# Kernel optimization log

Hardware: AMD Instinct MI355X
Metric: run time of the kernel (lower is better)

The kernel has to match this reference:

```python
import jax, jax.numpy as jnp
import numpy as np

B, S, D, H = 4, 1024, 1024, 16
HS = D // H  # head_size = 64


def setup_inputs() -> dict:
    key = jax.random.key(0)
    ks = jax.random.split(key, 12)
    sc_d = 1.0 / np.sqrt(D)
    sc_h = 1.0 / np.sqrt(HS)
    inp = {
        "queries": jax.random.normal(ks[0], (B, S, D), jnp.float32),
        "keys": jax.random.normal(ks[1], (B, S, D), jnp.float32),
        "values": jax.random.normal(ks[2], (B, S, D), jnp.float32),
        # causal mask: scores where mask == 0 are filled with -1e9
        "mask": jnp.tril(jnp.ones((S, S), jnp.int32)),
        # per-head query/key projections: [H, D, HS] weights, [H, HS] biases
        "Wq": jax.random.uniform(ks[3], (H, D, HS), jnp.float32, -sc_d, sc_d),
        "bq": jax.random.uniform(ks[4], (H, HS), jnp.float32, -sc_d, sc_d),
        "Wk": jax.random.uniform(ks[5], (H, D, HS), jnp.float32, -sc_d, sc_d),
        "bk": jax.random.uniform(ks[6], (H, HS), jnp.float32, -sc_d, sc_d),
        # shared value projection: [D, HS]
        "Wv": jax.random.uniform(ks[7], (D, HS), jnp.float32, -sc_d, sc_d),
        "bv": jax.random.uniform(ks[8], (HS,), jnp.float32, -sc_d, sc_d),
        # output projection: [HS, D]
        "Wo": jax.random.uniform(ks[9], (HS, D), jnp.float32, -sc_h, sc_h),
        "bo": jax.random.uniform(ks[10], (D,), jnp.float32, -sc_h, sc_h),
    }
    return inp


def reference(queries, keys, values, mask, Wq, bq, Wk, bk, Wv, bv, Wo, bo):
    # shared value projection: [B, S, HS]
    v = jnp.einsum("bsd,de->bse", values, Wv) + bv
    # batched per-head projections (replaces the python loop over heads)
    q = jnp.einsum("bsd,hde->bhse", queries, Wq) + bq[None, :, None, :]
    k = jnp.einsum("btd,hde->bhte", keys, Wk) + bk[None, :, None, :]
    scores = jnp.einsum("bhse,bhte->bhst", q, k) / jnp.sqrt(jnp.float32(HS))
    scores = jnp.where(mask == 0, jnp.float32(-1e9), scores)
    attn = jax.nn.softmax(scores, axis=-1)  # [B, H, S, S]; dropout = eval-mode identity
    head_out = jnp.einsum("bhst,bte->bhse", attn, v)
    out = head_out.mean(axis=1)  # mean over heads -> [B, S, HS]
    out = jnp.einsum("bse,ed->bsd", out, Wo) + bo
    attention_weights = attn.mean(axis=1)  # [B, S, S]
    return out, attention_weights
```

## Files before the change

kernel.cpp:

```cpp
#include <hip/hip_runtime.h>
#include <hip/hip_bf16.h>
#include <stdint.h>

typedef _Float16 half8 __attribute__((ext_vector_type(8)));
typedef _Float16 half4 __attribute__((ext_vector_type(4)));
typedef float    f32x4 __attribute__((ext_vector_type(4)));

#define MFMA16(a, b, c) __builtin_amdgcn_mfma_f32_16x16x32_f16(a, b, c, 0, 0, 0)

typedef __attribute__((address_space(1))) const void GVOID;
typedef __attribute__((address_space(3))) void LVOID;
__device__ __forceinline__ void glds16(const void* g, void* l)
{
    __builtin_amdgcn_global_load_lds((GVOID*)g, (LVOID*)l, 16, 0, 0);
}

#define BARRIER() do { asm volatile("" ::: "memory"); \
    __builtin_amdgcn_s_barrier(); \
    asm volatile("" ::: "memory"); } while (0)

__global__ __launch_bounds__(256) void prep_all(
    const float* __restrict__ Wq, const float* __restrict__ Wk,
    const float* __restrict__ Wv, const float* __restrict__ Wo,
    const float* __restrict__ queries, const float* __restrict__ keys,
    _Float16* __restrict__ WqkT, _Float16* __restrict__ WvT,
    _Float16* __restrict__ WoT, _Float16* __restrict__ a16,
    float* __restrict__ ctx, float* __restrict__ attn)
{
    __shared__ float t[32][33];
    const int id = blockIdx.x;
    const int tid = threadIdx.x;

    if (id < 2176) {
        const float* X; _Float16* Y; int R, C, bx, by;
        if (id < 2048) {
            const int isK = id >> 10;
            const int local = id & 1023;
            bx = local & 1;
            by = (local >> 1) & 31;
            const int hz = local >> 6;
            X = (isK ? Wk : Wq) + (long)hz * 65536;
            Y = WqkT + (long)isK * 1048576 + (long)hz * 65536;
            R = 1024; C = 64;
        } else if (id < 2112) {
            const int local = id - 2048;
            bx = local & 1; by = local >> 1;
            X = Wv; Y = WvT; R = 1024; C = 64;
        } else {
            const int local = id - 2112;
            bx = local & 31; by = local >> 5;
            X = Wo; Y = WoT; R = 64; C = 1024;
        }
        const int c0 = bx * 32, r0 = by * 32;
        const int tx = tid & 31, ty = tid >> 5;
#pragma unroll
        for (int i = 0; i < 4; ++i)
            t[ty + i * 8][tx] = X[(long)(r0 + ty + i * 8) * C + c0 + tx];
        __syncthreads();
#pragma unroll
        for (int i = 0; i < 4; ++i)
            Y[(long)(c0 + ty + i * 8) * R + r0 + tx] = (_Float16)t[tx][ty + i * 8];
    } else if (id < 6272) {
        const int isK = (id - 2176) >> 11;
        const int local = (id - 2176) & 2047;
        const float* S = isK ? keys : queries;
        _Float16* Dz = a16 + (long)isK * 4194304;
        const long i = ((long)local * 256 + tid) * 8;
        const float4 v0 = *(const float4*)(S + i);
        const float4 v1 = *(const float4*)(S + i + 4);
        half8 h;
        h[0] = (_Float16)v0.x; h[1] = (_Float16)v0.y;
        h[2] = (_Float16)v0.z; h[3] = (_Float16)v0.w;
        h[4] = (_Float16)v1.x; h[5] = (_Float16)v1.y;
        h[6] = (_Float16)v1.z; h[7] = (_Float16)v1.w;
        *(half8*)(Dz + i) = h;
    } else if (id < 6528) {
        const float4 z = {0.f, 0.f, 0.f, 0.f};
        ((float4*)ctx)[(long)(id - 6272) * 256 + tid] = z;
    } else {
        const float4 z = {0.f, 0.f, 0.f, 0.f};
        ((float4*)attn)[(long)(id - 6528) * 256 + tid] = z;
    }
}

__global__ __launch_bounds__(256, 2) void qk_vproj(
    const _Float16* __restrict__ A16,
    const _Float16* __restrict__ BT,
    const float* __restrict__ bias0, const float* __restrict__ bias1,
    _Float16* __restrict__ Cout,
    const float* __restrict__ values,
    const _Float16* __restrict__ WvT,
    const float* __restrict__ bv,
    _Float16* __restrict__ vT)
{
    __shared__ __align__(16) char smem[65536];
    const int lid = blockIdx.x;
    const int tid = threadIdx.x;
    const int wave = tid >> 6, lane = tid & 63;
    const int m16  = lane & 15, quad = lane >> 4;

    if (lid < 32) {
        _Float16 (*As)[72] = (_Float16(*)[72])smem;
        _Float16 (*Bs)[72] = (_Float16(*)[72])(smem + 128 * 72 * 2);
        const int mt = lid;
        const int m0 = mt * 128;

        const int acol = (tid & 15) * 4;
        const int arb  = tid >> 4;
        const int bj   = tid >> 1;
        const int bcc  = (tid & 1) * 32;
        const int jn = (bj > 63) ? 63 : bj;
        const _Float16* bpB = WvT + (long)jn * 1024;

        f32x4 acc[2][8];
        {
            f32x4 zz = {0.f, 0.f, 0.f, 0.f};
#pragma unroll
            for (int i = 0; i < 2; ++i)
#pragma unroll
                for (int j = 0; j < 8; ++j) acc[i][j] = zz;
        }

        for (int k0 = 0; k0 < 1024; k0 += 64) {
            {
                float4 av[8];
#pragma unroll
                for (int p = 0; p < 8; ++p)
                    av[p] = *(const float4*)(values + (long)(m0 + arb + p * 16) * 1024 + k0 + acol);
#pragma unroll
                for (int p = 0; p < 8; ++p) {
                    half4 hv;
                    hv[0] = (_Float16)av[p].x; hv[1] = (_Float16)av[p].y;
                    hv[2] = (_Float16)av[p].z; hv[3] = (_Float16)av[p].w;
                    *(half4*)&As[arb + p * 16][acol] = hv;
                }
            }
            {
                const _Float16* bp = bpB + k0 + bcc;
                half8 b0 = *(const half8*)(bp);
                half8 b1 = *(const half8*)(bp + 8);
                half8 b2 = *(const half8*)(bp + 16);
                half8 b3 = *(const half8*)(bp + 24);
                *(half8*)&Bs[bj][bcc]      = b0;
                *(half8*)&Bs[bj][bcc + 8]  = b1;
                *(half8*)&Bs[bj][bcc + 16] = b2;
                *(half8*)&Bs[bj][bcc + 24] = b3;
            }
            __syncthreads();
#pragma unroll
            for (int kss = 0; kss < 2; ++kss) {
                const int ko = kss * 32 + quad * 8;
                const half8 a0 = *(const half8*)&As[wave * 32 + m16][ko];
                const half8 a1 = *(const half8*)&As[wave * 32 + 16 + m16][ko];
#pragma unroll
                for (int c = 0; c < 4; ++c) {
                    const half8 bf = *(const half8*)&Bs[c * 16 + m16][ko];
                    acc[0][c] = MFMA16(a0, bf, acc[0][c]);
                    acc[1][c] = MFMA16(a1, bf, acc[1][c]);
                }
            }
            __syncthreads();
        }

#pragma unroll
        for (int hh = 0; hh < 2; ++hh) {
#pragma unroll
            for (int c = 0; c < 4; ++c) {
                const int e  = c * 16 + m16;
                const float bb = bv[e];
#pragma unroll
                for (int r = 0; r < 4; ++r) {
                    const int row = m0 + wave * 32 + hh * 16 + quad * 4 + r;
                    const int b = row >> 10, tt = row & 1023;
                    vT[(long)b * 65536 + (long)e * 1024 + tt] =
                        (_Float16)(acc[hh][c][r] + bb);
                }
            }
        }
        return;
    }

    const int lid2 = lid - 32;
    const int xcd = lid2 & 7, loc = lid2 >> 3;
    const int sw  = xcd * 64 + loc;
    const int nt  = sw & 7;
    const int tm2 = sw >> 3;
    const int mt  = tm2 & 31;
    const int z   = tm2 >> 5;

    const int n0 = nt * 128;
    const int m0 = mt * 128;

    const char* Az = (const char*)(A16 + (long)z * 4194304);
    const char* Bz = (const char*)(BT  + (long)z * 1048576);

    const int colbyte = (((lane & 7) ^ (lane >> 3)) << 4);
    const char* gaBase = Az + ((long)(m0 + wave * 32 + (lane >> 3)) << 11) + colbyte;
    const char* gbBase = Bz + ((long)(n0 + wave * 32 + (lane >> 3)) << 11) + colbyte;

    f32x4 acc[2][8];
    {
        f32x4 zz = {0.f, 0.f, 0.f, 0.f};
#pragma unroll
        for (int i = 0; i < 2; ++i)
#pragma unroll
            for (int j = 0; j < 8; ++j) acc[i][j] = zz;
    }

    auto STAGE = [&](int bf, int k0) {
        const char* ga = gaBase + (k0 << 1);
        const char* gb = gbBase + (k0 << 1);
        _Float16* la = (_Float16*)(smem + bf * 16384) + wave * 32 * 64;
        _Float16* lb = (_Float16*)(smem + 32768 + bf * 16384) + wave * 32 * 64;
#pragma unroll
        for (int i = 0; i < 4; ++i) {
            glds16(ga + (long)i * 8 * 2048, la + i * 8 * 64);
            glds16(gb + (long)i * 8 * 2048, lb + i * 8 * 64);
        }
    };

    auto COMPUTE = [&](int bf) {
        const char* Ab = smem + bf * 16384;
        const char* Bp = smem + 32768 + bf * 16384;
        const int sw4 = (m16 & 7) << 4;
#pragma unroll
        for (int kss = 0; kss < 2; ++kss) {
            const int kbs = (kss * 64 + quad * 16) ^ sw4;
            const half8 a0 = *(const half8*)(Ab + (wave * 32 + m16) * 128 + kbs);
            const half8 a1 = *(const half8*)(Ab + (wave * 32 + 16 + m16) * 128 + kbs);
#pragma unroll
            for (int c = 0; c < 8; ++c) {
                const half8 bfr = *(const half8*)(Bp + (c * 16 + m16) * 128 + kbs);
                acc[0][c] = MFMA16(a0, bfr, acc[0][c]);
                acc[1][c] = MFMA16(a1, bfr, acc[1][c]);
            }
        }
    };

    STAGE(0, 0);
    STAGE(1, 64);
    int cur = 0;
    for (int t = 0; t < 15; ++t) {
        asm volatile("s_waitcnt vmcnt(8)" ::: "memory");
        __builtin_amdgcn_sched_barrier(0);
        BARRIER();
        COMPUTE(cur);
        BARRIER();
        if (t < 14) STAGE(cur, (t + 2) * 64);
        cur ^= 1;
    }
    asm volatile("s_waitcnt vmcnt(0)" ::: "memory");
    __builtin_amdgcn_sched_barrier(0);
    BARRIER();
    COMPUTE(cur);

    const float* bias = z ? bias1 : bias0;
    _Float16* Cz = Cout + (long)z * 4194304;
#pragma unroll
    for (int hh = 0; hh < 2; ++hh) {
#pragma unroll
        for (int c = 0; c < 8; ++c) {
            const int col = n0 + c * 16 + m16;
            const float bb = bias[col];
#pragma unroll
            for (int r = 0; r < 4; ++r) {
                const int row = m0 + wave * 32 + hh * 16 + quad * 4 + r;
                Cz[(long)row * 1024 + col] = (_Float16)(acc[hh][c][r] + bb);
            }
        }
    }
}

__global__ __launch_bounds__(256, 2) void gemm_f16_v2(
    const float* __restrict__ A0, const float* __restrict__ A1,
    const _Float16* __restrict__ BT,
    const float* __restrict__ bias0, const float* __restrict__ bias1,
    void* __restrict__ Cout,
    int N, int lda, int ldbt, int ldc,
    long aBS, long bBS, long cBS,
    int c_half, int atomic, int nks, int kchunk)
{
    __shared__ __align__(16) _Float16 As[128][72];
    __shared__ __align__(16) _Float16 Bs[128][72];

    const int gx  = gridDim.x, gy = gridDim.y;
    const int nwg = gx * gy * (int)gridDim.z;
    const int lid = (int)blockIdx.x + gx * ((int)blockIdx.y + gy * (int)blockIdx.z);
    const int q8  = nwg >> 3, r8 = nwg & 7;
    const int xcd = lid & 7, loc = lid >> 3;
    const int sw  = (xcd < r8 ? xcd * (q8 + 1) : r8 * (q8 + 1) + (xcd - r8) * q8) + loc;
    const int nt  = sw % gx;
    const int tm2 = sw / gx;
    const int mt  = tm2 % gy;
    const int bz  = tm2 / gy;

    const int b = bz / nks, ks = bz % nks;
    const int kbeg = ks * kchunk;
    const int kend = kbeg + kchunk;

    const float* A = A1 ? (b ? A1 : A0) : (A0 + (long)b * aBS);
    const _Float16* Bb = BT + (long)b * bBS;

    const int n0 = nt * 128;
    const int m0 = mt * 128;
    const int tid  = threadIdx.x;
    const int wave = tid >> 6, lane = tid & 63;
    const int m16  = lane & 15, quad = lane >> 4;

    const int acol = (tid & 15) * 4;
    const int arb  = tid >> 4;
    const int bj   = tid >> 1;
    const int bcc  = (tid & 1) * 32;
    int jn = n0 + bj; if (jn > N - 1) jn = N - 1;
    const _Float16* bpB = Bb + (long)jn * ldbt;

    f32x4 acc[2][8];
    {
        f32x4 zz = {0.f, 0.f, 0.f, 0.f};
#pragma unroll
        for (int i = 0; i < 2; ++i)
#pragma unroll
            for (int j = 0; j < 8; ++j) acc[i][j] = zz;
    }

    for (int k0 = kbeg; k0 < kend; k0 += 64) {
        {
            float4 av[8];
#pragma unroll
            for (int p = 0; p < 8; ++p)
                av[p] = *(const float4*)(A + (long)(m0 + arb + p * 16) * lda + k0 + acol);
#pragma unroll
            for (int p = 0; p < 8; ++p) {
                half4 hv;
                hv[0] = (_Float16)av[p].x; hv[1] = (_Float16)av[p].y;
                hv[2] = (_Float16)av[p].z; hv[3] = (_Float16)av[p].w;
                *(half4*)&As[arb + p * 16][acol] = hv;
            }
        }
        {
            const _Float16* bp = bpB + k0 + bcc;
            half8 b0 = *(const half8*)(bp);
            half8 b1 = *(const half8*)(bp + 8);
            half8 b2 = *(const half8*)(bp + 16);
            half8 b3 = *(const half8*)(bp + 24);
            *(half8*)&Bs[bj][bcc]      = b0;
            *(half8*)&Bs[bj][bcc + 8]  = b1;
            *(half8*)&Bs[bj][bcc + 16] = b2;
            *(half8*)&Bs[bj][bcc + 24] = b3;
        }
        __syncthreads();
#pragma unroll
        for (int kss = 0; kss < 2; ++kss) {
            const int ko = kss * 32 + quad * 8;
            const half8 a0 = *(const half8*)&As[wave * 32 + m16][ko];
            const half8 a1 = *(const half8*)&As[wave * 32 + 16 + m16][ko];
#pragma unroll
            for (int c = 0; c < 8; ++c) {
                const half8 bf = *(const half8*)&Bs[c * 16 + m16][ko];
                acc[0][c] = MFMA16(a0, bf, acc[0][c]);
                acc[1][c] = MFMA16(a1, bf, acc[1][c]);
            }
        }
        __syncthreads();
    }

    const float* bias = b ? bias1 : bias0;
    const int addb = (bias != nullptr) && (kbeg == 0);
#pragma unroll
    for (int hh = 0; hh < 2; ++hh) {
#pragma unroll
        for (int c = 0; c < 8; ++c) {
            const int col = n0 + c * 16 + m16;
            if (col >= N) continue;
            const float bb = addb ? bias[col] : 0.f;
#pragma unroll
            for (int r = 0; r < 4; ++r) {
                const int row = m0 + wave * 32 + hh * 16 + quad * 4 + r;
                const float v = acc[hh][c][r] + bb;
                const long idx = (long)b * cBS + (long)row * ldc + col;
                if (atomic)      atomicAdd(&((float*)Cout)[idx], v);
                else if (c_half) ((_Float16*)Cout)[idx] = (_Float16)v;
                else             ((float*)Cout)[idx] = v;
            }
        }
    }
}

__global__ __launch_bounds__(256, 4) void attn_stats(
    const _Float16* __restrict__ q_all, const _Float16* __restrict__ k_all,
    float* __restrict__ m_out, float* __restrict__ il_out)
{
    const int st = blockIdx.x, h = blockIdx.y, b = blockIdx.z;
    const int tid = threadIdx.x, wave = tid >> 6, lane = tid & 63;
    const int m16 = lane & 15, quad = lane >> 4;
    const int s0 = st * 64;
    const int sw = s0 + wave * 16;

    __shared__ __align__(16) _Float16 qs[64][72];
    __shared__ __align__(16) _Float16 ks[128][72];

    const int srow = tid >> 2;
    const int scol = (tid & 3) * 16;

    {
        const _Float16* qsrc = q_all + ((long)(b * 1024 + s0 + srow)) * 1024 + h * 64 + scol;
        *(half8*)&qs[srow][scol]     = *(const half8*)(qsrc);
        *(half8*)&qs[srow][scol + 8] = *(const half8*)(qsrc + 8);
    }

    const _Float16* ksrcb = k_all + ((long)(b * 1024 + srow)) * 1024 + h * 64 + scol;

    float mr[4], lr[4];
#pragma unroll
    for (int r = 0; r < 4; ++r) { mr[r] = -3.0e38f; lr[r] = 0.f; }

    half8 a0, a1;
    for (int ch = 0; 2 * ch <= st; ++ch) {
        const int tbase = 2 * ch;
        const int two = (tbase + 1 <= st);

        const _Float16* ksrc0 = ksrcb + (long)(tbase * 64) * 1024;
        const half8 k0 = *(const half8*)(ksrc0);
        const half8 k1 = *(const half8*)(ksrc0 + 8);
        half8 k2, k3;
        if (two) {
            const _Float16* ksrc1 = ksrc0 + (long)64 * 1024;
            k2 = *(const half8*)(ksrc1);
            k3 = *(const half8*)(ksrc1 + 8);
        }

        __syncthreads();
        *(half8*)&ks[srow][scol]     = k0;
        *(half8*)&ks[srow][scol + 8] = k1;
        if (two) {
            *(half8*)&ks[64 + srow][scol]     = k2;
            *(half8*)&ks[64 + srow][scol + 8] = k3;
        }
        __syncthreads();

        if (ch == 0) {
            a0 = *(const half8*)&qs[wave * 16 + m16][quad * 8];
            a1 = *(const half8*)&qs[wave * 16 + m16][quad * 8 + 32];
        }

        const int ncol = two ? 8 : 4;
        for (int c = 0; c < ncol; ++c) {
            const half8 b0 = *(const half8*)&ks[c * 16 + m16][quad * 8];
            const half8 b1 = *(const half8*)&ks[c * 16 + m16][quad * 8 + 32];
            f32x4 cc = {0.f, 0.f, 0.f, 0.f};
            cc = MFMA16(a0, b0, cc);
            cc = MFMA16(a1, b1, cc);
            const int tile = tbase + (c >> 2);
            if (tile < st) {
#pragma unroll
                for (int r = 0; r < 4; ++r) {
                    const float zz = cc[r] * 0.125f;
                    const float nm = fmaxf(mr[r], zz);
                    lr[r] = lr[r] * __expf(mr[r] - nm) + __expf(zz - nm);
                    mr[r] = nm;
                }
            } else {
                const int col = tile * 64 + (c & 3) * 16 + m16;
#pragma unroll
                for (int r = 0; r < 4; ++r) {
                    const int row = sw + quad * 4 + r;
                    if (col <= row) {
                        const float zz = cc[r] * 0.125f;
                        const float nm = fmaxf(mr[r], zz);
                        lr[r] = lr[r] * __expf(mr[r] - nm) + __expf(zz - nm);
                        mr[r] = nm;
                    }
                }
            }
        }
    }

#pragma unroll
    for (int mk = 1; mk < 16; mk <<= 1) {
#pragma unroll
        for (int r = 0; r < 4; ++r) {
            const float om = __shfl_xor(mr[r], mk);
            const float ol = __shfl_xor(lr[r], mk);
            const float nm = fmaxf(mr[r], om);
            lr[r] = lr[r] * __expf(mr[r] - nm) + ol * __expf(om - nm);
            mr[r] = nm;
        }
    }
    if (m16 == 0) {
#pragma unroll
        for (int r = 0; r < 4; ++r) {
            const long idx = ((long)(b * 16 + h)) * 1024 + sw + quad * 4 + r;
            m_out[idx]  = mr[r];
            il_out[idx] = 1.f / lr[r];
        }
    }
}

__global__ __launch_bounds__(256, 4) void attn_pmean(
    const _Float16* __restrict__ q_all, const _Float16* __restrict__ k_all,
    const float* __restrict__ m_in, const float* __restrict__ il_in,
    const _Float16* __restrict__ vT,
    float* __restrict__ attn,
    float* __restrict__ ctx)
{
    const int ttile = blockIdx.x, stile = blockIdx.y, b = blockIdx.z;
    const int tid = threadIdx.x;
    if (ttile > stile) return;

    __shared__ __align__(16) _Float16 qs2[2][64 * 64];
    __shared__ __align__(16) _Float16 ks2[2][64 * 64];
    __shared__ __align__(16) float mls[16][64];
    __shared__ __align__(16) float ils[16][64];

    const int wave = tid >> 6, lane = tid & 63;
    const int m16 = lane & 15, quad = lane >> 4;
    const int s0 = stile * 64;
    const int t0 = ttile * 64;
    const int sw = s0 + wave * 16;
    const int diag = (ttile == stile);

    {
        const int hh = tid >> 4;
        const int c4 = (tid & 15) * 4;
        const long ix = ((long)(b * 16 + hh)) * 1024 + s0 + c4;
        const float4 mv4 = *(const float4*)&m_in[ix];
        const float4 iv4 = *(const float4*)&il_in[ix];
        *(float4*)&mls[hh][c4] = mv4;
        *(float4*)&ils[hh][c4] = iv4;
    }

    const int colb = (((lane & 7) ^ (lane >> 3)) << 4);
    const char* gq = (const char*)q_all + ((long)(b * 1024 + s0 + wave * 16 + (lane >> 3)) << 11) + colb;
    const char* gk = (const char*)k_all + ((long)(b * 1024 + t0 + wave * 16 + (lane >> 3)) << 11) + colb;

    auto STAGE_P = [&](int bf, int h) {
        const char* q = gq + h * 128;
        const char* k = gk + h * 128;
        _Float16* lq = &qs2[bf][wave * 16 * 64];
        _Float16* lk = &ks2[bf][wave * 16 * 64];
        glds16(q, lq);
        glds16(q + 8 * 2048, lq + 8 * 64);
        glds16(k, lk);
        glds16(k + 8 * 2048, lk + 8 * 64);
    };

    STAGE_P(0, 0);
    STAGE_P(1, 1);
    asm volatile("s_waitcnt lgkmcnt(0)" ::: "memory");
    BARRIER();

    float pm[4][4];
#pragma unroll
    for (int c = 0; c < 4; ++c)
#pragma unroll
        for (int r = 0; r < 4; ++r) pm[c][r] = 0.f;

    const int swz = (m16 & 7) << 4;
    int cur = 0;

    auto COMPUTE_H = [&](int h, int bf) {
        const char* Qc = (const char*)&qs2[bf][0];
        const char* Kc = (const char*)&ks2[bf][0];
        const half8 a0 = *(const half8*)(Qc + (wave * 16 + m16) * 128 + ((quad * 16) ^ swz));
        const half8 a1 = *(const half8*)(Qc + (wave * 16 + m16) * 128 + ((quad * 16 + 64) ^ swz));
        const float4 mv = *(const float4*)&mls[h][wave * 16 + quad * 4];
        const float4 iv = *(const float4*)&ils[h][wave * 16 + quad * 4];
        const float mrow[4] = {mv.x, mv.y, mv.z, mv.w};
        const float irow[4] = {iv.x, iv.y, iv.z, iv.w};
        if (!diag) {
#pragma unroll
            for (int c = 0; c < 4; ++c) {
                const half8 b0 = *(const half8*)(Kc + (c * 16 + m16) * 128 + ((quad * 16) ^ swz));
                const half8 b1 = *(const half8*)(Kc + (c * 16 + m16) * 128 + ((quad * 16 + 64) ^ swz));
                f32x4 cc = {0.f, 0.f, 0.f, 0.f};
                cc = MFMA16(a0, b0, cc);
                cc = MFMA16(a1, b1, cc);
#pragma unroll
                for (int r = 0; r < 4; ++r)
                    pm[c][r] += __expf(cc[r] * 0.125f - mrow[r]) * irow[r];
            }
        } else {
#pragma unroll
            for (int c = 0; c < 4; ++c) {
                const half8 b0 = *(const half8*)(Kc + (c * 16 + m16) * 128 + ((quad * 16) ^ swz));
                const half8 b1 = *(const half8*)(Kc + (c * 16 + m16) * 128 + ((quad * 16 + 64) ^ swz));
                f32x4 cc = {0.f, 0.f, 0.f, 0.f};
                cc = MFMA16(a0, b0, cc);
                cc = MFMA16(a1, b1, cc);
                const int col = t0 + c * 16 + m16;
#pragma unroll
                for (int r = 0; r < 4; ++r) {
                    const int row = sw + quad * 4 + r;
                    if (col <= row)
                        pm[c][r] += __expf(cc[r] * 0.125f - mrow[r]) * irow[r];
                }
            }
        }
    };

    for (int h = 0; h < 15; ++h) {
        asm volatile("s_waitcnt vmcnt(4)" ::: "memory");
        __builtin_amdgcn_sched_barrier(0);
        BARRIER();
        COMPUTE_H(h, cur);
        BARRIER();
        if (h < 14) STAGE_P(cur, h + 2);
        cur ^= 1;
    }
    asm volatile("s_waitcnt vmcnt(0)" ::: "memory");
    __builtin_amdgcn_sched_barrier(0);
    BARRIER();
    COMPUTE_H(15, cur);
    __syncthreads();

    {
        char* Pb = (char*)&qs2[0][0];
#pragma unroll
        for (int c = 0; c < 4; ++c) {
#pragma unroll
            for (int r = 0; r < 4; ++r) {
                const int rloc = (wave << 4) + (quad << 2) + r;
                const int cloc = c * 16 + m16;
                const float p = pm[c][r] * 0.0625f;
                attn[((long)(b * 1024 + s0 + rloc)) * 1024 + t0 + cloc] = p;
                const int chunk = (cloc >> 3) ^ (rloc & 7);
                *(_Float16*)(Pb + rloc * 128 + (chunk << 4) + (cloc & 7) * 2) =
                    (_Float16)p;
            }
        }
    }
    __syncthreads();

    const _Float16* vTb = vT + (long)b * 65536 + t0;
    const char* Pb = (const char*)&qs2[0][0];
    const int Rr = wave * 16 + m16;
    f32x4 apv[4];
    {
        f32x4 zz = {0.f, 0.f, 0.f, 0.f};
#pragma unroll
        for (int c = 0; c < 4; ++c) apv[c] = zz;
    }
#pragma unroll
    for (int kss = 0; kss < 2; ++kss) {
        const int chunk = (kss * 4 + quad) ^ (Rr & 7);
        const half8 a = *(const half8*)(Pb + Rr * 128 + (chunk << 4));
#pragma unroll
        for (int c = 0; c < 4; ++c) {
            const half8 bf = *(const half8*)(vTb + (long)(c * 16 + m16) * 1024 + kss * 32 + quad * 8);
            apv[c] = MFMA16(a, bf, apv[c]);
        }
    }
#pragma unroll
    for (int c = 0; c < 4; ++c) {
#pragma unroll
        for (int r = 0; r < 4; ++r) {
            const int row = sw + quad * 4 + r;
            const int e   = c * 16 + m16;
            atomicAdd(&ctx[((long)(b * 1024 + row)) * 64 + e], apv[c][r]);
        }
    }
}

extern "C" void kernel_launch(void* const* d_in, const int* in_sizes, int n_in,
                              void* d_out, int out_size, void* d_ws, size_t ws_size,
                              hipStream_t stream)
{
    const float* queries = (const float*)d_in[0];
    const float* keys    = (const float*)d_in[1];
    const float* values  = (const float*)d_in[2];
    const float* Wq = (const float*)d_in[4];
    const float* bq = (const float*)d_in[5];
    const float* Wk = (const float*)d_in[6];
    const float* bk = (const float*)d_in[7];
    const float* Wv = (const float*)d_in[8];
    const float* bv = (const float*)d_in[9];
    const float* Wo = (const float*)d_in[10];
    const float* bo = (const float*)d_in[11];

    float* out_ptr  = (float*)d_out;
    float* attn_ptr = out_ptr + (long)4096 * 1024;

    uint8_t* w = (uint8_t*)d_ws;
    size_t off = 0;
    auto alloc = [&](size_t bytes) {
        void* p = w + off;
        off = (off + bytes + 255) & ~(size_t)255;
        return p;
    };
    _Float16* WqkT  = (_Float16*)alloc((size_t)2 * 1024 * 1024 * 2);
    _Float16* WvT   = (_Float16*)alloc((size_t)64 * 1024 * 2);
    _Float16* WoT   = (_Float16*)alloc((size_t)1024 * 64 * 2);
    _Float16* qkall = (_Float16*)alloc((size_t)2 * 4194304 * 2);
    _Float16* a16   = (_Float16*)alloc((size_t)2 * 4194304 * 2);
    _Float16* vT    = (_Float16*)alloc((size_t)4 * 64 * 1024 * 2);
    float*    ctx   = (float*)alloc((size_t)4096 * 64 * 4);
    float*    mbuf  = (float*)alloc((size_t)65536 * 4);
    float*    ilbuf = (float*)alloc((size_t)65536 * 4);
    (void)ws_size; (void)in_sizes; (void)n_in; (void)out_size;

    _Float16* qall = qkall;
    _Float16* kall = qkall + (long)4194304;

    prep_all<<<dim3(10624, 1, 1), 256, 0, stream>>>(
        Wq, Wk, Wv, Wo, queries, keys,
        WqkT, WvT, WoT, a16, ctx, attn_ptr);

    qk_vproj<<<dim3(544, 1, 1), 256, 0, stream>>>(
        a16, WqkT, bq, bk, qkall, values, WvT, bv, vT);

    attn_stats<<<dim3(16, 16, 4), 256, 0, stream>>>(qall, kall, mbuf, ilbuf);

    attn_pmean<<<dim3(16, 16, 4), 256, 0, stream>>>(qall, kall, mbuf, ilbuf, vT, attn_ptr, ctx);

    gemm_f16_v2<<<dim3(8, 32, 1), 256, 0, stream>>>(
        ctx, nullptr, WoT, bo, nullptr, out_ptr,
        1024, 64, 64, 1024,
        0, 0, 0,
        0, 0, 1, 64);
}
```

Baseline: 229.8 us.

## Zero only masked attention tiles in-kernel and simplify QK projection pipeline

The separate full zero-fill of the attention-weights output in the prep kernel is removed. Instead, the blocks of attn_pmean that early-exit on upper-triangle tiles now write zeros for their own tiles, so lower-triangle tiles are no longer written twice. The QK projection GEMM drops its double-buffered global-to-LDS pipeline for a single buffer and shrinks LDS use, so its launch bound can raise occupancy to four blocks per CU. That trades explicit load/compute overlap for more resident waves hiding latency.

```diff
diff --git a/kernel.cpp b/kernel.cpp
--- a/kernel.cpp
+++ b/kernel.cpp
@@ -25,7 +25,7 @@
     const float* __restrict__ queries, const float* __restrict__ keys,
     _Float16* __restrict__ WqkT, _Float16* __restrict__ WvT,
     _Float16* __restrict__ WoT, _Float16* __restrict__ a16,
-    float* __restrict__ ctx, float* __restrict__ attn)
+    float* __restrict__ ctx)
 {
     __shared__ float t[32][33];
     const int id = blockIdx.x;
@@ -74,16 +74,13 @@
         h[4] = (_Float16)v1.x; h[5] = (_Float16)v1.y;
         h[6] = (_Float16)v1.z; h[7] = (_Float16)v1.w;
         *(half8*)(Dz + i) = h;
-    } else if (id < 6528) {
+    } else {
         const float4 z = {0.f, 0.f, 0.f, 0.f};
         ((float4*)ctx)[(long)(id - 6272) * 256 + tid] = z;
-    } else {
-        const float4 z = {0.f, 0.f, 0.f, 0.f};
-        ((float4*)attn)[(long)(id - 6528) * 256 + tid] = z;
     }
 }
 
-__global__ __launch_bounds__(256, 2) void qk_vproj(
+__global__ __launch_bounds__(256, 4) void qk_vproj(
     const _Float16* __restrict__ A16,
     const _Float16* __restrict__ BT,
     const float* __restrict__ bias0, const float* __restrict__ bias1,
@@ -93,17 +90,16 @@
     const float* __restrict__ bv,
     _Float16* __restrict__ vT)
 {
-    __shared__ __align__(16) char smem[65536];
+    __shared__ __align__(16) char smem[34816];
     const int lid = blockIdx.x;
     const int tid = threadIdx.x;
     const int wave = tid >> 6, lane = tid & 63;
     const int m16  = lane & 15, quad = lane >> 4;
 
     if (lid < 32) {
-        _Float16 (*As)[72] = (_Float16(*)[72])smem;
-        _Float16 (*Bs)[72] = (_Float16(*)[72])(smem + 128 * 72 * 2);
-        const int mt = lid;
-        const int m0 = mt * 128;
+        _Float16 (*As)[68] = (_Float16(*)[68])smem;
+        _Float16 (*Bs)[68] = (_Float16(*)[68])(smem + 17408);
+        const int m0 = lid * 128;
 
         const int acol = (tid & 15) * 4;
         const int arb  = tid >> 4;
@@ -112,13 +108,13 @@
         const int jn = (bj > 63) ? 63 : bj;
         const _Float16* bpB = WvT + (long)jn * 1024;
 
-        f32x4 acc[2][8];
+        f32x4 acc[2][4];
         {
             f32x4 zz = {0.f, 0.f, 0.f, 0.f};
 #pragma unroll
             for (int i = 0; i < 2; ++i)
 #pragma unroll
-                for (int j = 0; j < 8; ++j) acc[i][j] = zz;
+                for (int j = 0; j < 4; ++j) acc[i][j] = zz;
         }
 
         for (int k0 = 0; k0 < 1024; k0 += 64) {
@@ -207,52 +203,42 @@
             for (int j = 0; j < 8; ++j) acc[i][j] = zz;
     }
 
-    auto STAGE = [&](int bf, int k0) {
-        const char* ga = gaBase + (k0 << 1);
-        const char* gb = gbBase + (k0 << 1);
-        _Float16* la = (_Float16*)(smem + bf * 16384) + wave * 32 * 64;
-        _Float16* lb = (_Float16*)(smem + 32768 + bf * 16384) + wave * 32 * 64;
-#pragma unroll
-        for (int i = 0; i < 4; ++i) {
-            glds16(ga + (long)i * 8 * 2048, la + i * 8 * 64);
-            glds16(gb + (long)i * 8 * 2048, lb + i * 8 * 64);
-        }
-    };
-
-    auto COMPUTE = [&](int bf) {
-        const char* Ab = smem + bf * 16384;
-        const char* Bp = smem + 32768 + bf * 16384;
-        const int sw4 = (m16 & 7) << 4;
-#pragma unroll
-        for (int kss = 0; kss < 2; ++kss) {
-            const int kbs = (kss * 64 + quad * 16) ^ sw4;
-            const half8 a0 = *(const half8*)(Ab + (wave * 32 + m16) * 128 + kbs);
-            const half8 a1 = *(const half8*)(Ab + (wave * 32 + 16 + m16) * 128 + kbs);
-#pragma unroll
-            for (int c = 0; c < 8; ++c) {
-                const half8 bfr = *(const half8*)(Bp + (c * 16 + m16) * 128 + kbs);
-                acc[0][c] = MFMA16(a0, bfr, acc[0][c]);
-                acc[1][c] = MFMA16(a1, bfr, acc[1][c]);
-            }
-        }
-    };
-
-    STAGE(0, 0);
-    STAGE(1, 64);
-    int cur = 0;
-    for (int t = 0; t < 15; ++t) {
-        asm volatile("s_waitcnt vmcnt(8)" ::: "memory");
-        __builtin_amdgcn_sched_barrier(0);
-        BARRIER();
-        COMPUTE(cur);
-        BARRIER();
-        if (t < 14) STAGE(cur, (t + 2) * 64);
-        cur ^= 1;
-    }
-    asm volatile("s_waitcnt vmcnt(0)" ::: "memory");
-    __builtin_amdgcn_sched_barrier(0);
-    BARRIER();
-    COMPUTE(cur);
+    _Float16* As = (_Float16*)smem;
+    _Float16* Bs = (_Float16*)(smem + 16384);
+
+    for (int t = 0; t < 16; ++t) {
+        const int k0 = t * 64;
+        {
+            const char* ga = gaBase + (k0 << 1);
+            const char* gb = gbBase + (k0 << 1);
+            _Float16* la = As + wave * 32 * 64;
+            _Float16* lb = Bs + wave * 32 * 64;
+#pragma unroll
+            for (int i = 0; i < 4; ++i) {
+                glds16(ga + (long)i * 8 * 2048, la + i * 8 * 64);
+                glds16(gb + (long)i * 8 * 2048, lb + i * 8 * 64);
+            }
+        }
+        __syncthreads();
+        {
+            const char* Ab = (const char*)As;
+            const char* Bp = (const char*)Bs;
+            const int sw4 = (m16 & 7) << 4;
+#pragma unroll
+            for (int kss = 0; kss < 2; ++kss) {
+                const int kbs = (kss * 64 + quad * 16) ^ sw4;
+                const half8 a0 = *(const half8*)(Ab + (wave * 32 + m16) * 128 + kbs);
+                const half8 a1 = *(const half8*)(Ab + (wave * 32 + 16 + m16) * 128 + kbs);
+#pragma unroll
+                for (int c = 0; c < 8; ++c) {
+                    const half8 bfr = *(const half8*)(Bp + (c * 16 + m16) * 128 + kbs);
+                    acc[0][c] = MFMA16(a0, bfr, acc[0][c]);
+                    acc[1][c] = MFMA16(a1, bfr, acc[1][c]);
+                }
+            }
+        }
+        __syncthreads();
+    }
 
     const float* bias = z ? bias1 : bias0;
     _Float16* Cz = Cout + (long)z * 4194304;
@@ -505,7 +491,16 @@
 {
     const int ttile = blockIdx.x, stile = blockIdx.y, b = blockIdx.z;
     const int tid = threadIdx.x;
-    if (ttile > stile) return;
+    if (ttile > stile) {
+        const int c4 = (tid & 15) * 4;
+        float4 zz = {0.f, 0.f, 0.f, 0.f};
+#pragma unroll
+        for (int i = 0; i < 4; ++i) {
+            const int r = stile * 64 + (tid >> 4) + i * 16;
+            *(float4*)&attn[((long)(b * 1024 + r)) * 1024 + ttile * 64 + c4] = zz;
+        }
+        return;
+    }
 
     __shared__ __align__(16) _Float16 qs2[2][64 * 64];
     __shared__ __align__(16) _Float16 ks2[2][64 * 64];
@@ -701,9 +696,9 @@
     _Float16* qall = qkall;
     _Float16* kall = qkall + (long)4194304;
 
-    prep_all<<<dim3(10624, 1, 1), 256, 0, stream>>>(
+    prep_all<<<dim3(6528, 1, 1), 256, 0, stream>>>(
         Wq, Wk, Wv, Wo, queries, keys,
-        WqkT, WvT, WoT, a16, ctx, attn_ptr);
+        WqkT, WvT, WoT, a16, ctx);
 
     qk_vproj<<<dim3(544, 1, 1), 256, 0, stream>>>(
         a16, WqkT, bq, bk, qkall, values, WvT, bv, vT);
```

Measured after the change: 252.8 us. 1.1x slower.
